# Optimization experiments

Measured on AMD Instinct MI355X. Metric: run time of the kernel, lower is better.

Reference implementation:

```python
import jax, jax.numpy as jnp
import numpy as np

B, L, HID, NH, HD = 1, 2304, 3072, 24, 128
IMG = 2048
MLP = 4 * HID  # 12288
EPS = 1e-6


def _layernorm(x):
    mu = jnp.mean(x, axis=-1, keepdims=True)
    var = jnp.mean(jnp.square(x - mu), axis=-1, keepdims=True)
    return (x - mu) * jax.lax.rsqrt(var + EPS)


def _rmsnorm(x, w):
    ms = jnp.mean(jnp.square(x), axis=-1, keepdims=True)
    return x * jax.lax.rsqrt(ms + EPS) * w


def _rope_interleaved(x, cos, sin):
    # x: [B, S, H, D]; cos/sin: [1, S, 1, D] with pairwise-equal values (mode=1, GPT-J)
    x1 = x[..., 0::2]
    x2 = x[..., 1::2]
    c = cos[..., 0::2]
    s = sin[..., 0::2]
    even = x1 * c - x2 * s
    odd = x1 * s + x2 * c
    return jnp.stack([even, odd], axis=-1).reshape(x.shape)


def setup_inputs() -> dict:
    key = jax.random.key(0)
    ks = jax.random.split(key, 10)
    scale_in = 1.0 / np.sqrt(HID)
    x = jax.random.normal(ks[0], (B, L, HID), jnp.float32)
    vec = jax.random.normal(ks[1], (B, HID), jnp.float32)
    # RoPE tables (interleaved layout: value repeated per pair)
    pos = jnp.arange(IMG, dtype=jnp.float32)
    inv_freq = 1.0 / (10000.0 ** (jnp.arange(HD // 2, dtype=jnp.float32) / (HD // 2)))
    ang = pos[:, None] * inv_freq[None, :]               # [IMG, HD/2]
    freqs_cos = jnp.repeat(jnp.cos(ang), 2, axis=-1).reshape(1, IMG, 1, HD)
    freqs_sin = jnp.repeat(jnp.sin(ang), 2, axis=-1).reshape(1, IMG, 1, HD)
    mod_w = jax.random.normal(ks[2], (HID, 3 * HID), jnp.float32) * scale_in
    mod_b = jnp.zeros((3 * HID,), jnp.float32)
    w1 = jax.random.normal(ks[3], (HID, 3 * HID + MLP), jnp.float32) * scale_in
    b1 = jnp.zeros((3 * HID + MLP,), jnp.float32)
    q_norm_w = jnp.ones((HD,), jnp.float32)
    k_norm_w = jnp.ones((HD,), jnp.float32)
    w2 = jax.random.normal(ks[4], (HID + MLP, HID), jnp.float32) * (1.0 / np.sqrt(HID + MLP))
    b2 = jnp.zeros((HID,), jnp.float32)
    return {
        'x': x, 'vec': vec, 'img_len': IMG,
        'freqs_cos': freqs_cos, 'freqs_sin': freqs_sin,
        'mod_w': mod_w, 'mod_b': mod_b, 'w1': w1, 'b1': b1,
        'q_norm_w': q_norm_w, 'k_norm_w': k_norm_w, 'w2': w2, 'b2': b2,
    }


def reference(x, vec, img_len, freqs_cos, freqs_sin, mod_w, mod_b, w1, b1,
              q_norm_w, k_norm_w, w2, b2):
    # modulation: SiLU(vec) -> Linear -> shift/scale/gate  [B, HID] each
    mod = jax.nn.silu(vec) @ mod_w + mod_b
    shift, scale, gate = jnp.split(mod, 3, axis=-1)
    x_mod = _layernorm(x) * (1.0 + scale[:, None, :]) + shift[:, None, :]

    # fused QKV + MLP projection
    proj = x_mod @ w1 + b1                                  # [B, L, 3*HID + MLP]
    qkv, mlp = proj[..., :3 * HID], proj[..., 3 * HID:]
    q, k, v = [t[:, :, 0] for t in [None]] if False else None, None, None
    qkv = qkv.reshape(B, L, 3, NH, HD)
    q, k, v = qkv[:, :, 0], qkv[:, :, 1], qkv[:, :, 2]      # [B, L, NH, HD]

    q = _rmsnorm(q, q_norm_w)
    k = _rmsnorm(k, k_norm_w)

    # RoPE only on image tokens
    q = jnp.concatenate([_rope_interleaved(q[:, :img_len], freqs_cos, freqs_sin), q[:, img_len:]], axis=1)
    k = jnp.concatenate([_rope_interleaved(k[:, :img_len], freqs_cos, freqs_sin), k[:, img_len:]], axis=1)

    # full (img+txt) bidirectional attention
    attn_scale = 1.0 / np.sqrt(HD)
    scores = jnp.einsum('blhd,bmhd->bhlm', q, k) * attn_scale
    probs = jax.nn.softmax(scores, axis=-1)
    attn = jnp.einsum('bhlm,bmhd->blhd', probs, v).reshape(B, L, NH * HD)

    # output fusion: [attn | gelu_tanh(mlp)] @ w2
    out = jnp.concatenate([attn, jax.nn.gelu(mlp, approximate=True)], axis=-1) @ w2 + b2
    return x + out * gate[:, None, :]
```

## Files before the change

kernel.cpp:

```cpp
#include <hip/hip_runtime.h>

#define L_SEQ 2304
#define HID_D 3072
#define NH_D 24
#define HD_D 128
#define N1_D 21504
#define QKVN 9216
#define K2_D 15360
#define EPS_V 1e-6f
#define ATTN_SC 0.08838834764831843f

typedef __bf16 bf16x8 __attribute__((ext_vector_type(8)));
typedef float f32x4 __attribute__((ext_vector_type(4)));
typedef unsigned int u32x4 __attribute__((ext_vector_type(4)));
typedef unsigned short u16x8 __attribute__((ext_vector_type(8)));
typedef unsigned short u16x4 __attribute__((ext_vector_type(4)));

#define WAITVM(N) asm volatile("s_waitcnt vmcnt(" #N ")" ::: "memory")
#define LGKM0 asm volatile("s_waitcnt lgkmcnt(0)" ::: "memory")
#define SB0 __builtin_amdgcn_sched_barrier(0)

__device__ __forceinline__ unsigned short f2bf(float f) {
  unsigned int u = __builtin_bit_cast(unsigned int, f);
  u += 0x7fffu + ((u >> 16) & 1u);
  return (unsigned short)(u >> 16);
}
__device__ __forceinline__ float bf2f(unsigned short u) {
  return __builtin_bit_cast(float, (unsigned int)u << 16);
}

__device__ __forceinline__ float gelu_f(float x) {
  float u = 0.7978845608028654f * (x + 0.044715f * x * x * x);
  float e = __expf(2.f * u);
  float th = 1.f - 2.f / (e + 1.f);
  return 0.5f * x * (1.f + th);
}

__device__ __forceinline__ void gload16(const void* g, void* l) {
  __builtin_amdgcn_global_load_lds(
      (const __attribute__((address_space(1))) unsigned int*)g,
      (__attribute__((address_space(3))) unsigned int*)l, 16, 0, 0);
}

__global__ __launch_bounds__(256) void mod_partial_kernel(
    const float* __restrict__ vec, const float* __restrict__ mod_w,
    float* __restrict__ partial) {
  __shared__ float s[384];
  const int t = threadIdx.x;
  const int kb = blockIdx.y;
  const int k0 = kb * 384;
  for (int p = t; p < 384; p += 256) {
    float v = vec[k0 + p];
    s[p] = v / (1.f + __expf(-v));
  }
  __syncthreads();
  const int n = blockIdx.x * 256 + t;
  float acc = 0.f;
  const float* wp = mod_w + (size_t)k0 * QKVN + n;
#pragma unroll 4
  for (int j = 0; j < 384; ++j) acc += s[j] * wp[(size_t)j * QKVN];
  partial[kb * QKVN + n] = acc;
}

__global__ __launch_bounds__(256) void mod_reduce_kernel(
    const float* __restrict__ partial, const float* __restrict__ mod_b,
    float* __restrict__ mod) {
  const int n = blockIdx.x * 256 + threadIdx.x;
  float acc = mod_b[n];
#pragma unroll
  for (int i = 0; i < 8; ++i) acc += partial[i * QKVN + n];
  mod[n] = acc;
}

__global__ __launch_bounds__(256) void ln_mod_kernel(
    const float* __restrict__ x, const float* __restrict__ mod,
    unsigned short* __restrict__ xmod) {
  const int row = blockIdx.x;
  const int t = threadIdx.x;
  const float* xr = x + (size_t)row * HID_D;
  float4 v[3];
  float sum = 0.f, sq = 0.f;
#pragma unroll
  for (int p = 0; p < 3; ++p) {
    v[p] = *(const float4*)&xr[p * 1024 + t * 4];
    sum += v[p].x + v[p].y + v[p].z + v[p].w;
    sq += v[p].x * v[p].x + v[p].y * v[p].y + v[p].z * v[p].z + v[p].w * v[p].w;
  }
#pragma unroll
  for (int o = 1; o < 64; o <<= 1) {
    sum += __shfl_xor(sum, o);
    sq += __shfl_xor(sq, o);
  }
  __shared__ float rs[8];
  const int w = t >> 6;
  if ((t & 63) == 0) { rs[w] = sum; rs[4 + w] = sq; }
  __syncthreads();
  sum = rs[0] + rs[1] + rs[2] + rs[3];
  sq = rs[4] + rs[5] + rs[6] + rs[7];
  const float mu = sum * (1.f / HID_D);
  const float var = sq * (1.f / HID_D) - mu * mu;
  const float rstd = rsqrtf(var + EPS_V);
#pragma unroll
  for (int p = 0; p < 3; ++p) {
    const int c = p * 1024 + t * 4;
    float4 sc = *(const float4*)&mod[3072 + c];
    float4 sh = *(const float4*)&mod[c];
    u16x4 o4;
    o4[0] = f2bf((v[p].x - mu) * rstd * (1.f + sc.x) + sh.x);
    o4[1] = f2bf((v[p].y - mu) * rstd * (1.f + sc.y) + sh.y);
    o4[2] = f2bf((v[p].z - mu) * rstd * (1.f + sc.z) + sh.z);
    o4[3] = f2bf((v[p].w - mu) * rstd * (1.f + sc.w) + sh.w);
    *(u16x4*)&xmod[(size_t)row * HID_D + c] = o4;
  }
}

__global__ __launch_bounds__(256) void convert_transpose_kernel(
    const float* __restrict__ src, unsigned short* __restrict__ dst,
    const int K, const int N) {
  __shared__ unsigned short lt[64][72];
  const int t = threadIdx.x;
  const int n0 = blockIdx.x * 64;
  const int k0 = blockIdx.y * 64;
  const int kr = t >> 4;
  const int n4 = (t & 15) * 4;
#pragma unroll
  for (int p = 0; p < 4; ++p) {
    const int k = kr + p * 16;
    float4 v = *(const float4*)&src[(size_t)(k0 + k) * N + n0 + n4];
    lt[n4 + 0][k] = f2bf(v.x);
    lt[n4 + 1][k] = f2bf(v.y);
    lt[n4 + 2][k] = f2bf(v.z);
    lt[n4 + 3][k] = f2bf(v.w);
  }
  __syncthreads();
  const int nr = t >> 2;
  const int kc = (t & 3) * 16;
  u16x8 a = *(const u16x8*)&lt[nr][kc];
  u16x8 b = *(const u16x8*)&lt[nr][kc + 8];
  unsigned short* dp = &dst[(size_t)(n0 + nr) * K + k0 + kc];
  *(u16x8*)dp = a;
  *(u16x8*)(dp + 8) = b;
}

template <int BM>
__device__ __forceinline__ void gemm8_core(
    const unsigned short* __restrict__ A, const int lda,
    const unsigned short* __restrict__ B, const int ldb,
    const int m0, const int n0, const int nit, char* lds, f32x4 (*acc)[4]) {
  constexpr int AREG = (BM == 256) ? 16384 : 8192;
  constexpr int ABUF = 2 * AREG;
  constexpr int BOFF = 2 * ABUF;
  constexpr int BREG = 16384;
  constexpr int BBUF = 32768;
  constexpr int AROWS = (BM == 256) ? 128 : 64;
  constexpr int AI = (BM == 256) ? 2 : 1;
  constexpr int MF = (BM == 256) ? 4 : 2;
  constexpr int QM = (BM == 256) ? 64 : 32;

  const int t = threadIdx.x;
  const int lane = t & 63;
  const int w = t >> 6;
  const int g = lane >> 4;
  const int c = lane & 15;
  const int sr8 = lane >> 3;
  const int scol = ((lane & 7) ^ sr8) * 8;
  const int arg = w >> 2;
  const int brg = (w & 3) >> 1;
  const int bbase = (w & 1) * 64;

  auto stageA = [&](int buf, int rg, int kt) {
#pragma unroll
    for (int i = 0; i < AI; ++i)
      gload16(A + (size_t)(m0 + rg * AROWS + i * 64 + w * 8 + sr8) * lda +
                  kt * 64 + scol,
              lds + buf * ABUF + rg * AREG + i * 8192 + w * 1024);
  };
  auto stageB = [&](int buf, int rg, int kt) {
#pragma unroll
    for (int i = 0; i < 2; ++i)
      gload16(B + (size_t)(n0 + rg * 128 + i * 64 + w * 8 + sr8) * ldb +
                  kt * 64 + scol,
              lds + BOFF + buf * BBUF + rg * BREG + i * 8192 + w * 1024);
  };

  bf16x8 af[2 * MF], bq0[4], bq1[4];
  auto ldA = [&](int buf, int qm) {
    const char* ab = lds + buf * ABUF + arg * AREG;
#pragma unroll
    for (int i = 0; i < MF; ++i) {
      const int lr = qm * QM + i * 16 + c;
#pragma unroll
      for (int kk = 0; kk < 2; ++kk)
        af[i * 2 + kk] =
            *(const bf16x8*)(ab + lr * 128 + (((kk * 4 + g) ^ (c & 7)) << 4));
    }
  };
  auto ldB = [&](int buf, int qn, bf16x8* bq) {
    const char* bb = lds + BOFF + buf * BBUF + brg * BREG;
#pragma unroll
    for (int i = 0; i < 2; ++i) {
      const int lr = bbase + qn * 32 + i * 16 + c;
#pragma unroll
      for (int kk = 0; kk < 2; ++kk)
        bq[i * 2 + kk] =
            *(const bf16x8*)(bb + lr * 128 + (((kk * 4 + g) ^ (c & 7)) << 4));
    }
  };
  auto domf = [&](int qm, int qn, const bf16x8* bq) {
#pragma unroll
    for (int i = 0; i < MF; ++i)
#pragma unroll
      for (int n = 0; n < 2; ++n)
#pragma unroll
        for (int kk = 0; kk < 2; ++kk)
          acc[qm * MF + i][qn * 2 + n] = __builtin_amdgcn_mfma_f32_16x16x32_bf16(
              af[i * 2 + kk], bq[n * 2 + kk], acc[qm * MF + i][qn * 2 + n], 0, 0, 0);
  };
  auto MID = [&] {
    SB0;
    __builtin_amdgcn_s_barrier();
    LGKM0;
    SB0;
    __builtin_amdgcn_s_setprio(1);
  };
  auto END = [&] {
    __builtin_amdgcn_s_setprio(0);
    SB0;
    __builtin_amdgcn_s_barrier();
  };

  stageB(0, 0, 0); stageA(0, 0, 0); stageB(0, 1, 0); stageA(0, 1, 0);
  stageB(1, 0, 1); stageA(1, 0, 1);
  if constexpr (BM == 256) WAITVM(4); else WAITVM(3);
  __builtin_amdgcn_s_barrier();

  for (int j = 0; j < nit; ++j) {
    const int ta = 2 * j;
    const bool nl = (j + 1 < nit);
    ldA(0, 0); ldB(0, 0, bq0);
    stageB(1, 1, ta + 1);
    MID(); domf(0, 0, bq0); END();
    ldB(0, 1, bq1);
    stageA(1, 1, ta + 1);
    MID(); domf(0, 1, bq1); END();
    ldA(0, 1);
    if (nl) stageB(0, 0, ta + 2);
    MID(); domf(1, 1, bq1); END();
    if (nl) stageA(0, 0, ta + 2);
    MID(); domf(1, 0, bq0);
    __builtin_amdgcn_s_setprio(0); SB0;
    if (nl) { if constexpr (BM == 256) WAITVM(4); else WAITVM(3); }
    else WAITVM(0);
    __builtin_amdgcn_s_barrier();
    ldA(1, 0); ldB(1, 0, bq0);
    if (nl) stageB(0, 1, ta + 2);
    MID(); domf(0, 0, bq0); END();
    ldB(1, 1, bq1);
    if (nl) stageA(0, 1, ta + 2);
    MID(); domf(0, 1, bq1); END();
    ldA(1, 1);
    if (nl) stageB(1, 0, ta + 3);
    MID(); domf(1, 1, bq1); END();
    if (nl) stageA(1, 0, ta + 3);
    MID(); domf(1, 0, bq0);
    __builtin_amdgcn_s_setprio(0); SB0;
    if (nl) { if constexpr (BM == 256) WAITVM(4); else WAITVM(3); }
    __builtin_amdgcn_s_barrier();
  }
}

__global__ __launch_bounds__(512, 2) void gemm1_kernel(
    const unsigned short* __restrict__ xmod, const unsigned short* __restrict__ w1t,
    const float* __restrict__ b1, unsigned short* __restrict__ qkv,
    unsigned short* __restrict__ hbuf) {
  __shared__ __align__(16) char smem[131072];
  f32x4 acc[8][4];
  const f32x4 zero = {0.f, 0.f, 0.f, 0.f};
#pragma unroll
  for (int i = 0; i < 8; ++i)
#pragma unroll
    for (int j = 0; j < 4; ++j) acc[i][j] = zero;
  const int orig = blockIdx.x;
  const int xcd = orig & 7;
  const int wgid = (xcd < 4 ? xcd * 95 : 380 + (xcd - 4) * 94) + (orig >> 3);
  const int m0 = (wgid % 9) * 256;
  const int n0 = (wgid / 9) * 256;
  gemm8_core<256>(xmod, HID_D, w1t, HID_D, m0, n0, 24, smem, acc);
  const int lane = threadIdx.x & 63;
  const int g = lane >> 4, c = lane & 15;
  const int w = threadIdx.x >> 6;
  const int wm = (w >> 2) * 128, wn = (w & 3) * 64;
  const bool is_mlp = (n0 >= QKVN);
#pragma unroll
  for (int mf = 0; mf < 8; ++mf)
#pragma unroll
    for (int nf = 0; nf < 4; ++nf)
#pragma unroll
      for (int j = 0; j < 4; ++j) {
        const int row = m0 + wm + mf * 16 + g * 4 + j;
        const int col = n0 + wn + nf * 16 + c;
        const float v = acc[mf][nf][j] + b1[col];
        if (!is_mlp) {
          qkv[(size_t)row * QKVN + col] = f2bf(v);
        } else {
          hbuf[(size_t)row * K2_D + HID_D + (col - QKVN)] = f2bf(gelu_f(v));
        }
      }
}

__global__ __launch_bounds__(512, 2) void gemm2_kernel(
    const unsigned short* __restrict__ hbuf, const unsigned short* __restrict__ w2t,
    const float* __restrict__ b2, const float* __restrict__ x,
    const float* __restrict__ mod, float* __restrict__ out) {
  __shared__ __align__(16) char smem[98304];
  f32x4 acc[4][4];
  const f32x4 zero = {0.f, 0.f, 0.f, 0.f};
#pragma unroll
  for (int i = 0; i < 4; ++i)
#pragma unroll
    for (int j = 0; j < 4; ++j) acc[i][j] = zero;
  const int orig = blockIdx.x;
  const int wgid = (orig & 7) * 27 + (orig >> 3);
  const int m0 = (wgid % 18) * 128;
  const int n0 = (wgid / 18) * 256;
  gemm8_core<128>(hbuf, K2_D, w2t, K2_D, m0, n0, 120, smem, acc);
  const int lane = threadIdx.x & 63;
  const int g = lane >> 4, c = lane & 15;
  const int w = threadIdx.x >> 6;
  const int wm = (w >> 2) * 64, wn = (w & 3) * 64;
#pragma unroll
  for (int mf = 0; mf < 4; ++mf)
#pragma unroll
    for (int nf = 0; nf < 4; ++nf)
#pragma unroll
      for (int j = 0; j < 4; ++j) {
        const int row = m0 + wm + mf * 16 + g * 4 + j;
        const int col = n0 + wn + nf * 16 + c;
        const float v = acc[mf][nf][j] + b2[col];
        out[(size_t)row * HID_D + col] =
            x[(size_t)row * HID_D + col] + v * mod[6144 + col];
      }
}

__global__ __launch_bounds__(256) void qk_norm_rope_kernel(
    const unsigned short* __restrict__ qkv, const float* __restrict__ qw,
    const float* __restrict__ kw, const float* __restrict__ fc,
    const float* __restrict__ fs, const int* __restrict__ img_len_p,
    unsigned short* __restrict__ qr, unsigned short* __restrict__ kr) {
  const int l = blockIdx.x;
  const int t = threadIdx.x;
  const int wv = t >> 6;
  const int lane = t & 63;
  const int img = *img_len_p;
  const bool do_rope = (l < img);
  float cc = 1.f, ss = 0.f;
  if (do_rope) {
    cc = fc[l * HD_D + 2 * lane];
    ss = fs[l * HD_D + 2 * lane];
  }
  const float qw0 = qw[2 * lane], qw1 = qw[2 * lane + 1];
  const float kw0 = kw[2 * lane], kw1 = kw[2 * lane + 1];
#pragma unroll
  for (int hh = 0; hh < 6; ++hh) {
    const int h = hh * 4 + wv;
    {
      unsigned int pq = *(const unsigned int*)&qkv[(size_t)l * QKVN + h * HD_D + 2 * lane];
      float q0 = bf2f((unsigned short)(pq & 0xffff));
      float q1 = bf2f((unsigned short)(pq >> 16));
      float sq = q0 * q0 + q1 * q1;
#pragma unroll
      for (int o = 1; o < 64; o <<= 1) sq += __shfl_xor(sq, o);
      const float r = rsqrtf(sq * (1.f / HD_D) + EPS_V);
      float a = q0 * r * qw0, b = q1 * r * qw1;
      float e = a, od = b;
      if (do_rope) { e = a * cc - b * ss; od = a * ss + b * cc; }
      e *= ATTN_SC; od *= ATTN_SC;
      unsigned int pk = (unsigned)f2bf(e) | ((unsigned)f2bf(od) << 16);
      *(unsigned int*)&qr[((size_t)h * L_SEQ + l) * HD_D + 2 * lane] = pk;
    }
    {
      unsigned int pkk = *(const unsigned int*)&qkv[(size_t)l * QKVN + HID_D + h * HD_D + 2 * lane];
      float k0 = bf2f((unsigned short)(pkk & 0xffff));
      float k1 = bf2f((unsigned short)(pkk >> 16));
      float sq = k0 * k0 + k1 * k1;
#pragma unroll
      for (int o = 1; o < 64; o <<= 1) sq += __shfl_xor(sq, o);
      const float r = rsqrtf(sq * (1.f / HD_D) + EPS_V);
      float a = k0 * r * kw0, b = k1 * r * kw1;
      float e = a, od = b;
      if (do_rope) { e = a * cc - b * ss; od = a * ss + b * cc; }
      unsigned int pk = (unsigned)f2bf(e) | ((unsigned)f2bf(od) << 16);
      *(unsigned int*)&kr[((size_t)h * L_SEQ + l) * HD_D + 2 * lane] = pk;
    }
  }
}

__global__ __launch_bounds__(256) void v_transpose_kernel(
    const unsigned short* __restrict__ qkv, unsigned short* __restrict__ vT) {
  __shared__ unsigned short lv[128 * 64];
  const int h = blockIdx.y;
  const int l0 = blockIdx.x * 64;
  const int t = threadIdx.x;
#pragma unroll
  for (int p = 0; p < 4; ++p) {
    const int idx = p * 256 + t;
    const int l = idx >> 4;
    const int d8 = (idx & 15) * 8;
    u16x8 v = *(const u16x8*)&qkv[(size_t)(l0 + l) * QKVN + 2 * HID_D + h * HD_D + d8];
#pragma unroll
    for (int e = 0; e < 8; ++e) {
      const int d = d8 + e;
      const unsigned sw = (unsigned)(((d >> 2) & 7) << 4);
      *(unsigned short*)((char*)lv + (((unsigned)d * 128 + 2 * l) ^ sw)) = v[e];
    }
  }
  __syncthreads();
  const int d = t >> 1;
  const int half = t & 1;
  const unsigned swr = (unsigned)(((d >> 2) & 7) << 4);
#pragma unroll
  for (int j2 = 0; j2 < 4; ++j2) {
    u32x4 v = *(const u32x4*)((const char*)lv + ((d * 128 + half * 64 + j2 * 16) ^ swr));
    *(u32x4*)&vT[(size_t)(h * HD_D + d) * L_SEQ + l0 + half * 32 + j2 * 8] = v;
  }
}

__global__ __launch_bounds__(256) void attn_kernel(
    const unsigned short* __restrict__ qr, const unsigned short* __restrict__ kr,
    const unsigned short* __restrict__ vT, unsigned short* __restrict__ hbuf) {
  __shared__ unsigned short lds_k[64 * 128];
  __shared__ unsigned short lds_v[128 * 64];
  __shared__ unsigned short lds_p[4 * 16 * 64];
  const int hidx = blockIdx.y;
  const int l0 = blockIdx.x * 64;
  const int t = threadIdx.x;
  const int lane = t & 63;
  const int w = t >> 6;
  const int g = lane >> 4;
  const int c = lane & 15;

  bf16x8 qa[4];
  {
    const unsigned short* qrow = qr + ((size_t)hidx * L_SEQ + l0 + w * 16 + c) * HD_D;
#pragma unroll
    for (int ks = 0; ks < 4; ++ks)
      qa[ks] = *(const bf16x8*)&qrow[ks * 32 + g * 8];
  }
  f32x4 acc[8];
  const f32x4 zero = {0.f, 0.f, 0.f, 0.f};
#pragma unroll
  for (int i = 0; i < 8; ++i) acc[i] = zero;
  float m_r[4] = {-1e30f, -1e30f, -1e30f, -1e30f};
  float l_r[4] = {0.f, 0.f, 0.f, 0.f};

  u32x4 kreg[4], vreg[4];
  auto load_tile = [&](int kv0) {
#pragma unroll
    for (int p = 0; p < 4; ++p) {
      const int idx = p * 256 + t;
      const int r = idx >> 4, ch = idx & 15;
      kreg[p] = *(const u32x4*)&kr[((size_t)hidx * L_SEQ + kv0 + r) * HD_D + ch * 8];
    }
#pragma unroll
    for (int p = 0; p < 4; ++p) {
      const int idx = p * 256 + t;
      const int d_ = idx >> 3, ch = idx & 7;
      vreg[p] = *(const u32x4*)&vT[(size_t)(hidx * HD_D + d_) * L_SEQ + kv0 + ch * 8];
    }
  };
  load_tile(0);

  for (int kv0 = 0; kv0 < L_SEQ; kv0 += 64) {
    __syncthreads();
#pragma unroll
    for (int p = 0; p < 4; ++p) {
      const int idx = p * 256 + t;
      const int r = idx >> 4, ch = idx & 15;
      *(u32x4*)((char*)lds_k + ((r * 256 + ch * 16) ^ ((r & 7) << 4))) = kreg[p];
    }
#pragma unroll
    for (int p = 0; p < 4; ++p) {
      const int idx = p * 256 + t;
      const int d_ = idx >> 3, ch = idx & 7;
      *(u32x4*)((char*)lds_v + ((d_ * 128 + ch * 16) ^ ((d_ & 7) << 4))) = vreg[p];
    }
    __syncthreads();
    if (kv0 + 64 < L_SEQ) load_tile(kv0 + 64);
    f32x4 s[4];
#pragma unroll
    for (int cf = 0; cf < 4; ++cf) s[cf] = zero;
#pragma unroll
    for (int ks = 0; ks < 4; ++ks) {
      const int kb = (ks * 32 + g * 8) * 2;
#pragma unroll
      for (int cf = 0; cf < 4; ++cf) {
        const int kvr = cf * 16 + c;
        bf16x8 kf = *(const bf16x8*)((const char*)lds_k + ((kvr * 256 + kb) ^ ((kvr & 7) << 4)));
        s[cf] = __builtin_amdgcn_mfma_f32_16x16x32_bf16(qa[ks], kf, s[cf], 0, 0, 0);
      }
    }
    float pv[4][4];
    float alpha[4];
#pragma unroll
    for (int r = 0; r < 4; ++r) {
      float mx = fmaxf(fmaxf(s[0][r], s[1][r]), fmaxf(s[2][r], s[3][r]));
      mx = fmaxf(mx, __shfl_xor(mx, 1));
      mx = fmaxf(mx, __shfl_xor(mx, 2));
      mx = fmaxf(mx, __shfl_xor(mx, 4));
      mx = fmaxf(mx, __shfl_xor(mx, 8));
      const float mnew = fmaxf(m_r[r], mx);
      alpha[r] = __expf(m_r[r] - mnew);
      float rsum = 0.f;
#pragma unroll
      for (int cf = 0; cf < 4; ++cf) {
        const float p_ = __expf(s[cf][r] - mnew);
        pv[cf][r] = p_;
        rsum += p_;
      }
      rsum += __shfl_xor(rsum, 1);
      rsum += __shfl_xor(rsum, 2);
      rsum += __shfl_xor(rsum, 4);
      rsum += __shfl_xor(rsum, 8);
      l_r[r] = l_r[r] * alpha[r] + rsum;
      m_r[r] = mnew;
    }
#pragma unroll
    for (int of = 0; of < 8; ++of)
#pragma unroll
      for (int r = 0; r < 4; ++r) acc[of][r] *= alpha[r];
#pragma unroll
    for (int cf = 0; cf < 4; ++cf)
#pragma unroll
      for (int r = 0; r < 4; ++r) {
        const int row = g * 4 + r;
        const int col = cf * 16 + c;
        *(unsigned short*)((char*)lds_p +
                           ((w * 2048 + row * 128 + col * 2) ^ ((row & 7) << 4))) =
            f2bf(pv[cf][r]);
      }
    asm volatile("s_waitcnt lgkmcnt(0)" ::: "memory");
    __builtin_amdgcn_sched_barrier(0);
#pragma unroll
    for (int ks = 0; ks < 2; ++ks) {
      bf16x8 pa = *(const bf16x8*)((const char*)lds_p +
                                   ((w * 2048 + c * 128 + (ks * 32 + g * 8) * 2) ^
                                    ((c & 7) << 4)));
#pragma unroll
      for (int of = 0; of < 8; ++of) {
        const int dcol = of * 16 + c;
        bf16x8 vb = *(const bf16x8*)((const char*)lds_v +
                                     ((dcol * 128 + (ks * 32 + g * 8) * 2) ^
                                      ((dcol & 7) << 4)));
        acc[of] = __builtin_amdgcn_mfma_f32_16x16x32_bf16(pa, vb, acc[of], 0, 0, 0);
      }
    }
  }
  float rinv[4];
#pragma unroll
  for (int r = 0; r < 4; ++r) rinv[r] = 1.f / l_r[r];
#pragma unroll
  for (int of = 0; of < 8; ++of)
#pragma unroll
    for (int r = 0; r < 4; ++r) {
      const int row = l0 + w * 16 + g * 4 + r;
      const int col = hidx * HD_D + of * 16 + c;
      hbuf[(size_t)row * K2_D + col] = f2bf(acc[of][r] * rinv[r]);
    }
}

extern "C" void kernel_launch(void* const* d_in, const int* in_sizes, int n_in,
                              void* d_out, int out_size, void* d_ws, size_t ws_size,
                              hipStream_t stream) {
  (void)in_sizes; (void)n_in; (void)out_size; (void)ws_size;
  const float* x = (const float*)d_in[0];
  const float* vec = (const float*)d_in[1];
  const int* img_len = (const int*)d_in[2];
  const float* fc = (const float*)d_in[3];
  const float* fs = (const float*)d_in[4];
  const float* mod_w = (const float*)d_in[5];
  const float* mod_b = (const float*)d_in[6];
  const float* w1 = (const float*)d_in[7];
  const float* b1 = (const float*)d_in[8];
  const float* qw = (const float*)d_in[9];
  const float* kw = (const float*)d_in[10];
  const float* w2 = (const float*)d_in[11];
  const float* b2 = (const float*)d_in[12];
  float* out = (float*)d_out;

  char* wsb = (char*)d_ws;
  float* mod = (float*)(wsb + 0);
  float* partial = (float*)(wsb + 36864);
  unsigned short* xmod = (unsigned short*)(wsb + 331776);
  unsigned short* qkv = (unsigned short*)(wsb + 14487552);
  unsigned short* hbuf = (unsigned short*)(wsb + 99422208);
  unsigned short* qr = (unsigned short*)(wsb + 170201088);
  unsigned short* kr = (unsigned short*)(wsb + 184356864);
  unsigned short* vT = (unsigned short*)(wsb + 198512640);
  unsigned short* wt = (unsigned short*)(wsb + 212668416);

  mod_partial_kernel<<<dim3(36, 8), 256, 0, stream>>>(vec, mod_w, partial);
  mod_reduce_kernel<<<36, 256, 0, stream>>>(partial, mod_b, mod);
  ln_mod_kernel<<<2304, 256, 0, stream>>>(x, mod, xmod);
  convert_transpose_kernel<<<dim3(N1_D / 64, HID_D / 64), 256, 0, stream>>>(
      w1, wt, HID_D, N1_D);
  gemm1_kernel<<<756, 512, 0, stream>>>(xmod, wt, b1, qkv, hbuf);
  convert_transpose_kernel<<<dim3(HID_D / 64, K2_D / 64), 256, 0, stream>>>(
      w2, wt, K2_D, HID_D);
  qk_norm_rope_kernel<<<2304, 256, 0, stream>>>(qkv, qw, kw, fc, fs, img_len, qr, kr);
  v_transpose_kernel<<<dim3(36, 24), 256, 0, stream>>>(qkv, vT);
  attn_kernel<<<dim3(36, 24), 256, 0, stream>>>(qr, kr, vT, hbuf);
  gemm2_kernel<<<216, 512, 0, stream>>>(hbuf, wt, b2, x, mod, out);
}
```

Measured before the change: 957.3 us.

## Enlarge attention blocks to 128 queries with 8 waves and swizzled grid

The attention kernel now runs 512 threads per block, each block covering 128 query rows with 8 waves, so each K/V tile staged in LDS is shared by twice as many queries. The launch becomes a 1D grid of 432 blocks with a swizzle that maps blocks to (head, query-tile) pairs for better cache locality. The register prefetch of the next K/V tile is removed, and loads now go straight to LDS inside the loop. That cuts register pressure but exposes global load latency that the prefetch used to hide.

```diff
diff --git a/kernel.cpp b/kernel.cpp
--- a/kernel.cpp
+++ b/kernel.cpp
@@ -425,14 +425,16 @@
   }
 }
 
-__global__ __launch_bounds__(256) void attn_kernel(
+__global__ __launch_bounds__(512) void attn_kernel(
     const unsigned short* __restrict__ qr, const unsigned short* __restrict__ kr,
     const unsigned short* __restrict__ vT, unsigned short* __restrict__ hbuf) {
   __shared__ unsigned short lds_k[64 * 128];
   __shared__ unsigned short lds_v[128 * 64];
-  __shared__ unsigned short lds_p[4 * 16 * 64];
-  const int hidx = blockIdx.y;
-  const int l0 = blockIdx.x * 64;
+  __shared__ unsigned short lds_p[8 * 16 * 64];
+  const int bid = blockIdx.x;
+  const int swz = (bid & 7) * 54 + (bid >> 3);
+  const int hidx = swz / 18;
+  const int l0 = (swz % 18) * 128;
   const int t = threadIdx.x;
   const int lane = t & 63;
   const int w = t >> 6;
@@ -453,39 +455,23 @@
   float m_r[4] = {-1e30f, -1e30f, -1e30f, -1e30f};
   float l_r[4] = {0.f, 0.f, 0.f, 0.f};
 
-  u32x4 kreg[4], vreg[4];
-  auto load_tile = [&](int kv0) {
-#pragma unroll
-    for (int p = 0; p < 4; ++p) {
-      const int idx = p * 256 + t;
-      const int r = idx >> 4, ch = idx & 15;
-      kreg[p] = *(const u32x4*)&kr[((size_t)hidx * L_SEQ + kv0 + r) * HD_D + ch * 8];
-    }
-#pragma unroll
-    for (int p = 0; p < 4; ++p) {
-      const int idx = p * 256 + t;
-      const int d_ = idx >> 3, ch = idx & 7;
-      vreg[p] = *(const u32x4*)&vT[(size_t)(hidx * HD_D + d_) * L_SEQ + kv0 + ch * 8];
-    }
-  };
-  load_tile(0);
-
   for (int kv0 = 0; kv0 < L_SEQ; kv0 += 64) {
     __syncthreads();
 #pragma unroll
-    for (int p = 0; p < 4; ++p) {
-      const int idx = p * 256 + t;
+    for (int p = 0; p < 2; ++p) {
+      const int idx = p * 512 + t;
       const int r = idx >> 4, ch = idx & 15;
-      *(u32x4*)((char*)lds_k + ((r * 256 + ch * 16) ^ ((r & 7) << 4))) = kreg[p];
-    }
-#pragma unroll
-    for (int p = 0; p < 4; ++p) {
-      const int idx = p * 256 + t;
+      u32x4 v = *(const u32x4*)&kr[((size_t)hidx * L_SEQ + kv0 + r) * HD_D + ch * 8];
+      *(u32x4*)((char*)lds_k + ((r * 256 + ch * 16) ^ ((r & 7) << 4))) = v;
+    }
+#pragma unroll
+    for (int p = 0; p < 2; ++p) {
+      const int idx = p * 512 + t;
       const int d_ = idx >> 3, ch = idx & 7;
-      *(u32x4*)((char*)lds_v + ((d_ * 128 + ch * 16) ^ ((d_ & 7) << 4))) = vreg[p];
+      u32x4 v = *(const u32x4*)&vT[(size_t)(hidx * HD_D + d_) * L_SEQ + kv0 + ch * 8];
+      *(u32x4*)((char*)lds_v + ((d_ * 128 + ch * 16) ^ ((d_ & 7) << 4))) = v;
     }
     __syncthreads();
-    if (kv0 + 64 < L_SEQ) load_tile(kv0 + 64);
     f32x4 s[4];
 #pragma unroll
     for (int cf = 0; cf < 4; ++cf) s[cf] = zero;
@@ -608,6 +594,6 @@
       w2, wt, K2_D, HID_D);
   qk_norm_rope_kernel<<<2304, 256, 0, stream>>>(qkv, qw, kw, fc, fs, img_len, qr, kr);
   v_transpose_kernel<<<dim3(36, 24), 256, 0, stream>>>(qkv, vT);
-  attn_kernel<<<dim3(36, 24), 256, 0, stream>>>(qr, kr, vT, hbuf);
+  attn_kernel<<<432, 512, 0, stream>>>(qr, kr, vT, hbuf);
   gemm2_kernel<<<216, 512, 0, stream>>>(hbuf, wt, b2, x, mod, out);
 }
```

Result: no change. 946.1 us (-1.2%).

## Replace 8-phase GEMM pipeline with simpler 2-phase double buffer; drop attention KV prefetch

Applied to the files above, without the earlier changes.

The GEMM core is rewritten from an 8-phase schedule, which interleaved staging across two K-tiles per iteration, into a 2-phase double-buffered loop with one K-tile per iteration, so the iteration counts double. Loads for the next tile are issued in bulk before each half of the MFMA work. The attention kernel stops prefetching the next K/V tile into registers and instead loads straight into LDS between barriers. The intent is to cut barrier count and scheduling complexity, but it overlaps global loads with compute less and removes the attention load prefetch.

```diff
diff --git a/kernel.cpp b/kernel.cpp
--- a/kernel.cpp
+++ b/kernel.cpp
@@ -143,17 +143,16 @@
 }
 
 template <int BM>
-__device__ __forceinline__ void gemm8_core(
+__device__ __forceinline__ void gemm2p_core(
     const unsigned short* __restrict__ A, const int lda,
     const unsigned short* __restrict__ B, const int ldb,
-    const int m0, const int n0, const int nit, char* lds, f32x4 (*acc)[4]) {
+    const int m0, const int n0, const int nt, char* lds, f32x4 (*acc)[4]) {
   constexpr int AREG = (BM == 256) ? 16384 : 8192;
   constexpr int ABUF = 2 * AREG;
   constexpr int BOFF = 2 * ABUF;
   constexpr int BREG = 16384;
   constexpr int BBUF = 32768;
   constexpr int AROWS = (BM == 256) ? 128 : 64;
-  constexpr int AI = (BM == 256) ? 2 : 1;
   constexpr int MF = (BM == 256) ? 4 : 2;
   constexpr int QM = (BM == 256) ? 64 : 32;
 
@@ -168,19 +167,25 @@
   const int brg = (w & 3) >> 1;
   const int bbase = (w & 1) * 64;
 
-  auto stageA = [&](int buf, int rg, int kt) {
-#pragma unroll
-    for (int i = 0; i < AI; ++i)
-      gload16(A + (size_t)(m0 + rg * AROWS + i * 64 + w * 8 + sr8) * lda +
-                  kt * 64 + scol,
-              lds + buf * ABUF + rg * AREG + i * 8192 + w * 1024);
-  };
   auto stageB = [&](int buf, int rg, int kt) {
 #pragma unroll
     for (int i = 0; i < 2; ++i)
       gload16(B + (size_t)(n0 + rg * 128 + i * 64 + w * 8 + sr8) * ldb +
                   kt * 64 + scol,
               lds + BOFF + buf * BBUF + rg * BREG + i * 8192 + w * 1024);
+  };
+  auto stageAi = [&](int buf, int i, int kt) {
+#pragma unroll
+    for (int rg = 0; rg < 2; ++rg)
+      gload16(A + (size_t)(m0 + rg * AROWS + i * 64 + w * 8 + sr8) * lda +
+                  kt * 64 + scol,
+              lds + buf * ABUF + rg * AREG + i * 8192 + w * 1024);
+  };
+  auto stageA128 = [&](int buf, int kt) {
+#pragma unroll
+    for (int rg = 0; rg < 2; ++rg)
+      gload16(A + (size_t)(m0 + rg * AROWS + w * 8 + sr8) * lda + kt * 64 + scol,
+              lds + buf * ABUF + rg * AREG + w * 1024);
   };
 
   bf16x8 af[2 * MF], bq0[4], bq1[4];
@@ -223,48 +228,38 @@
     SB0;
     __builtin_amdgcn_s_setprio(1);
   };
-  auto END = [&] {
-    __builtin_amdgcn_s_setprio(0);
-    SB0;
+
+  if constexpr (BM == 256) {
+    stageB(0, 0, 0); stageB(0, 1, 0);
+    stageAi(0, 0, 0); stageAi(0, 1, 0);
+    WAITVM(2);
+  } else {
+    stageB(0, 0, 0); stageB(0, 1, 0); stageA128(0, 0);
+    WAITVM(0);
+  }
+  __builtin_amdgcn_s_barrier();
+
+  for (int j = 0; j < nt; ++j) {
+    const int b = j & 1;
+    const bool nl = (j + 1 < nt);
+    ldA(b, 0); ldB(b, 0, bq0); ldB(b, 1, bq1);
+    if (nl) {
+      stageB(b ^ 1, 0, j + 1); stageB(b ^ 1, 1, j + 1);
+      if constexpr (BM == 128) stageA128(b ^ 1, j + 1);
+    }
+    MID();
+    domf(0, 0, bq0); domf(0, 1, bq1);
+    __builtin_amdgcn_s_setprio(0); SB0;
+    if constexpr (BM == 256) { if (nl) WAITVM(4); else WAITVM(0); }
     __builtin_amdgcn_s_barrier();
-  };
-
-  stageB(0, 0, 0); stageA(0, 0, 0); stageB(0, 1, 0); stageA(0, 1, 0);
-  stageB(1, 0, 1); stageA(1, 0, 1);
-  if constexpr (BM == 256) WAITVM(4); else WAITVM(3);
-  __builtin_amdgcn_s_barrier();
-
-  for (int j = 0; j < nit; ++j) {
-    const int ta = 2 * j;
-    const bool nl = (j + 1 < nit);
-    ldA(0, 0); ldB(0, 0, bq0);
-    stageB(1, 1, ta + 1);
-    MID(); domf(0, 0, bq0); END();
-    ldB(0, 1, bq1);
-    stageA(1, 1, ta + 1);
-    MID(); domf(0, 1, bq1); END();
-    ldA(0, 1);
-    if (nl) stageB(0, 0, ta + 2);
-    MID(); domf(1, 1, bq1); END();
-    if (nl) stageA(0, 0, ta + 2);
-    MID(); domf(1, 0, bq0);
+    ldA(b, 1);
+    if constexpr (BM == 256) {
+      if (nl) { stageAi(b ^ 1, 0, j + 1); stageAi(b ^ 1, 1, j + 1); }
+    }
+    MID();
+    domf(1, 1, bq1); domf(1, 0, bq0);
     __builtin_amdgcn_s_setprio(0); SB0;
-    if (nl) { if constexpr (BM == 256) WAITVM(4); else WAITVM(3); }
-    else WAITVM(0);
-    __builtin_amdgcn_s_barrier();
-    ldA(1, 0); ldB(1, 0, bq0);
-    if (nl) stageB(0, 1, ta + 2);
-    MID(); domf(0, 0, bq0); END();
-    ldB(1, 1, bq1);
-    if (nl) stageA(0, 1, ta + 2);
-    MID(); domf(0, 1, bq1); END();
-    ldA(1, 1);
-    if (nl) stageB(1, 0, ta + 3);
-    MID(); domf(1, 1, bq1); END();
-    if (nl) stageA(1, 0, ta + 3);
-    MID(); domf(1, 0, bq0);
-    __builtin_amdgcn_s_setprio(0); SB0;
-    if (nl) { if constexpr (BM == 256) WAITVM(4); else WAITVM(3); }
+    if (nl) { if constexpr (BM == 256) WAITVM(2); else WAITVM(0); }
     __builtin_amdgcn_s_barrier();
   }
 }
@@ -285,7 +280,7 @@
   const int wgid = (xcd < 4 ? xcd * 95 : 380 + (xcd - 4) * 94) + (orig >> 3);
   const int m0 = (wgid % 9) * 256;
   const int n0 = (wgid / 9) * 256;
-  gemm8_core<256>(xmod, HID_D, w1t, HID_D, m0, n0, 24, smem, acc);
+  gemm2p_core<256>(xmod, HID_D, w1t, HID_D, m0, n0, 48, smem, acc);
   const int lane = threadIdx.x & 63;
   const int g = lane >> 4, c = lane & 15;
   const int w = threadIdx.x >> 6;
@@ -323,7 +318,7 @@
   const int wgid = (orig & 7) * 27 + (orig >> 3);
   const int m0 = (wgid % 18) * 128;
   const int n0 = (wgid / 18) * 256;
-  gemm8_core<128>(hbuf, K2_D, w2t, K2_D, m0, n0, 120, smem, acc);
+  gemm2p_core<128>(hbuf, K2_D, w2t, K2_D, m0, n0, 240, smem, acc);
   const int lane = threadIdx.x & 63;
   const int g = lane >> 4, c = lane & 15;
   const int w = threadIdx.x >> 6;
@@ -453,39 +448,23 @@
   float m_r[4] = {-1e30f, -1e30f, -1e30f, -1e30f};
   float l_r[4] = {0.f, 0.f, 0.f, 0.f};
 
-  u32x4 kreg[4], vreg[4];
-  auto load_tile = [&](int kv0) {
+  for (int kv0 = 0; kv0 < L_SEQ; kv0 += 64) {
+    __syncthreads();
 #pragma unroll
     for (int p = 0; p < 4; ++p) {
       const int idx = p * 256 + t;
       const int r = idx >> 4, ch = idx & 15;
-      kreg[p] = *(const u32x4*)&kr[((size_t)hidx * L_SEQ + kv0 + r) * HD_D + ch * 8];
+      u32x4 v = *(const u32x4*)&kr[((size_t)hidx * L_SEQ + kv0 + r) * HD_D + ch * 8];
+      *(u32x4*)((char*)lds_k + ((r * 256 + ch * 16) ^ ((r & 7) << 4))) = v;
     }
 #pragma unroll
     for (int p = 0; p < 4; ++p) {
       const int idx = p * 256 + t;
       const int d_ = idx >> 3, ch = idx & 7;
-      vreg[p] = *(const u32x4*)&vT[(size_t)(hidx * HD_D + d_) * L_SEQ + kv0 + ch * 8];
-    }
-  };
-  load_tile(0);
-
-  for (int kv0 = 0; kv0 < L_SEQ; kv0 += 64) {
+      u32x4 v = *(const u32x4*)&vT[(size_t)(hidx * HD_D + d_) * L_SEQ + kv0 + ch * 8];
+      *(u32x4*)((char*)lds_v + ((d_ * 128 + ch * 16) ^ ((d_ & 7) << 4))) = v;
+    }
     __syncthreads();
-#pragma unroll
-    for (int p = 0; p < 4; ++p) {
-      const int idx = p * 256 + t;
-      const int r = idx >> 4, ch = idx & 15;
-      *(u32x4*)((char*)lds_k + ((r * 256 + ch * 16) ^ ((r & 7) << 4))) = kreg[p];
-    }
-#pragma unroll
-    for (int p = 0; p < 4; ++p) {
-      const int idx = p * 256 + t;
-      const int d_ = idx >> 3, ch = idx & 7;
-      *(u32x4*)((char*)lds_v + ((d_ * 128 + ch * 16) ^ ((d_ & 7) << 4))) = vreg[p];
-    }
-    __syncthreads();
-    if (kv0 + 64 < L_SEQ) load_tile(kv0 + 64);
     f32x4 s[4];
 #pragma unroll
     for (int cf = 0; cf < 4; ++cf) s[cf] = zero;
```

New measurement: 1.038 ms. 8.4% more time.
